# Performance work log

Hardware: AMD Instinct MI355X
Metric: run time of the kernel (lower is better)

Reference implementation:

```python
import jax, jax.numpy as jnp
import numpy as np

N_NODES = 50000
N_EDGES = 1600000
HIDDEN = 128
N_RBF = 50


def _linear_init(key, fan_in, fan_out):
    # mimic torch nn.Linear default init: U(-1/sqrt(fan_in), 1/sqrt(fan_in))
    kw, kb = jax.random.split(key)
    bound = 1.0 / np.sqrt(fan_in)
    W = jax.random.uniform(kw, (fan_in, fan_out), minval=-bound, maxval=bound, dtype=jnp.float32)
    b = jax.random.uniform(kb, (fan_out,), minval=-bound, maxval=bound, dtype=jnp.float32)
    return W, b


def setup_inputs() -> dict:
    key = jax.random.key(0)
    ks = jax.random.split(key, 9)
    x = jax.random.normal(ks[0], (N_NODES, HIDDEN), dtype=jnp.float32)
    edge_index = jax.random.randint(ks[1], (2, N_EDGES), 0, N_NODES, dtype=jnp.int32)
    edge_attr = jax.random.uniform(ks[2], (N_EDGES, N_RBF), dtype=jnp.float32)
    fW1, fb1 = _linear_init(ks[3], N_RBF, HIDDEN)
    fW2, fb2 = _linear_init(ks[4], HIDDEN, HIDDEN)
    dW, db = _linear_init(ks[5], HIDDEN, HIDDEN)
    uW1, ub1 = _linear_init(ks[6], HIDDEN, HIDDEN)
    uW2, ub2 = _linear_init(ks[7], HIDDEN, HIDDEN)
    return {
        "x": x, "edge_index": edge_index, "edge_attr": edge_attr,
        "fW1": fW1, "fb1": fb1, "fW2": fW2, "fb2": fb2,
        "dW": dW, "db": db,
        "uW1": uW1, "ub1": ub1, "uW2": uW2, "ub2": ub2,
    }


def reference(x, edge_index, edge_attr, fW1, fb1, fW2, fb2, dW, db, uW1, ub1, uW2, ub2):
    src, dst = edge_index[0], edge_index[1]
    # filter network: Linear -> SiLU -> Linear on edge RBF features [E, n_rbf] -> [E, H]
    filters = jax.nn.silu(edge_attr @ fW1 + fb1) @ fW2 + fb2
    # messages: dense(x[src]) * filters  [E, H]
    messages = (x[src] @ dW + db) * filters
    # scatter-add to destination nodes
    aggregated = jax.ops.segment_sum(messages, dst, num_segments=x.shape[0])
    # update MLP + residual
    upd = jax.nn.silu(aggregated @ uW1 + ub1) @ uW2 + ub2
    return x + upd
```

## Files before the change

### kernel.cpp

```cpp
#include <hip/hip_runtime.h>

#define H    128
#define RBF  50
#define K1   64
#define EB   64
#define NB   32
#define NBLK 1024

typedef _Float16 f16;
typedef _Float16 f16x8 __attribute__((ext_vector_type(8)));
typedef float    f32x4 __attribute__((ext_vector_type(4)));

#define HS_LD 136

__device__ __forceinline__ float silu_f(float a) {
    return a / (1.0f + __expf(-a));
}


__global__ __launch_bounds__(256) void prep1_kernel(
    const float* __restrict__ x, const float* __restrict__ dW,
    const float* __restrict__ db, f16* __restrict__ h, int N, int nH,
    const float* __restrict__ fW1, const float* __restrict__ fW2,
    f16* __restrict__ Wt1, f16* __restrict__ Wt2,
    const int* __restrict__ dst, int* __restrict__ counts, int E)
{
    __shared__ float xs[NB][H];
    const int tid = threadIdx.x;
    const int b   = blockIdx.x;

    if (b < nH) {
        const int n0 = b * NB;
        for (int idx = tid; idx < NB * H; idx += 256) {
            int r = idx >> 7, c = idx & (H - 1);
            int n = n0 + r;
            xs[r][c] = (n < N) ? x[(size_t)n * H + c] : 0.f;
        }
        __syncthreads();
        const int j  = tid & (H - 1);
        const int rb = (tid >> 7) * 16;
        float acc[16];
        const float bb = db[j];
#pragma unroll
        for (int r = 0; r < 16; ++r) acc[r] = bb;
        for (int kq = 0; kq < H / 4; ++kq) {
            const int k = kq * 4;
            const float w0 = dW[(k + 0) * H + j];
            const float w1 = dW[(k + 1) * H + j];
            const float w2 = dW[(k + 2) * H + j];
            const float w3 = dW[(k + 3) * H + j];
#pragma unroll
            for (int r = 0; r < 16; ++r) {
                const float4 v = *(const float4*)&xs[rb + r][k];
                acc[r] = fmaf(v.x, w0, fmaf(v.y, w1, fmaf(v.z, w2, fmaf(v.w, w3, acc[r]))));
            }
        }
#pragma unroll
        for (int r = 0; r < 16; ++r) {
            int n = n0 + rb + r;
            if (n < N) h[(size_t)n * H + j] = (f16)acc[r];
        }
    } else if (b < nH + 96) {
        int i = (b - nH) * 256 + tid;
        if (i < H * K1) {
            int n = i >> 6, k = i & (K1 - 1);
            Wt1[i] = (k < RBF) ? (f16)fW1[k * H + n] : (f16)0.f;
        }
        int jj = i - H * K1;
        if (jj >= 0 && jj < H * H) {
            int n = jj >> 7, k = jj & (H - 1);
            Wt2[jj] = (f16)fW2[k * H + n];
        }
    } else {
        const int hb  = b - nH - 96;
        const int hgd = gridDim.x - nH - 96;
        for (int i = hb * 256 + tid; i < E; i += hgd * 256)
            atomicAdd(&counts[dst[i]], 1);
    }
}


__global__ __launch_bounds__(256) void scan1_kernel(
    const int* __restrict__ counts, int* __restrict__ ofs, int* __restrict__ bsum, int N)
{
    __shared__ int s[256];
    const int t = threadIdx.x;
    const int g = blockIdx.x * 256 + t;
    int v = (g < N) ? counts[g] : 0;
    s[t] = v; __syncthreads();
    for (int off = 1; off < 256; off <<= 1) {
        int u = 0; if (t >= off) u = s[t - off];
        __syncthreads(); s[t] += u; __syncthreads();
    }
    if (g < N) ofs[g] = s[t] - v;
    if (t == 255) bsum[blockIdx.x] = s[255];
}
__global__ __launch_bounds__(256) void scan2_kernel(int* __restrict__ bsum, int nb)
{
    __shared__ int s[256];
    const int t = threadIdx.x;
    int v = (t < nb) ? bsum[t] : 0;
    s[t] = v; __syncthreads();
    for (int off = 1; off < 256; off <<= 1) {
        int u = 0; if (t >= off) u = s[t - off];
        __syncthreads(); s[t] += u; __syncthreads();
    }
    if (t < nb) bsum[t] = s[t] - v;
}
__global__ __launch_bounds__(256) void scan3_kernel(
    int* __restrict__ ofs, int* __restrict__ cursor, const int* __restrict__ bsum, int N)
{
    int g = blockIdx.x * 256 + threadIdx.x;
    if (g < N) {
        int v = ofs[g] + bsum[blockIdx.x];
        ofs[g] = v;
        cursor[g] = v;
    }
}

__global__ __launch_bounds__(256) void ranges_kernel(
    const int* __restrict__ ofs, int* __restrict__ nstart, int* __restrict__ estart,
    int N, int E, int B)
{
    int b = blockIdx.x * 256 + threadIdx.x;
    if (b > B) return;
    if (b == B) { nstart[B] = N; estart[B] = E; return; }
    long long cb = (long long)b * E / B;
    int lo = 0, hi = N;
    while (lo < hi) {
        int mid = (lo + hi) >> 1;
        int val = (mid < N) ? ofs[mid] : E;
        if (val < (int)cb) lo = mid + 1; else hi = mid;
    }
    nstart[b] = lo;
    estart[b] = (lo < N) ? ofs[lo] : E;
}

__global__ __launch_bounds__(256) void build_kernel(
    const float* __restrict__ ea, const int* __restrict__ src, const int* __restrict__ dst,
    int* __restrict__ cursor, int2* __restrict__ sd, f16* __restrict__ ea16, int E)
{
    for (int e = blockIdx.x * 256 + threadIdx.x; e < E; e += gridDim.x * 256) {
        const int d = dst[e];
        const int pos = atomicAdd(&cursor[d], 1);
        sd[pos] = make_int2(src[e], d);

        const float* rp = ea + (size_t)e * RBF;
        f16* op = ea16 + (size_t)pos * K1;
        f16x8 v[8];
#pragma unroll
        for (int q = 0; q < 6; ++q) {
            const float4 a = *(const float4*)(rp + q * 8);
            const float4 b = *(const float4*)(rp + q * 8 + 4);
            f16x8 t;
            t[0]=(f16)a.x; t[1]=(f16)a.y; t[2]=(f16)a.z; t[3]=(f16)a.w;
            t[4]=(f16)b.x; t[5]=(f16)b.y; t[6]=(f16)b.z; t[7]=(f16)b.w;
            v[q] = t;
        }
        {
            const float2 a = *(const float2*)(rp + 48);
            f16x8 t = {};
            t[0]=(f16)a.x; t[1]=(f16)a.y;
            v[6] = t;
        }
        v[7] = (f16x8){};
#pragma unroll
        for (int q = 0; q < 8; ++q) *(f16x8*)(op + q * 8) = v[q];
    }
}

__global__ __launch_bounds__(256, 4) void edge_fused_kernel(
    const f16* __restrict__ ea16, const int2* __restrict__ sd,
    const f16* __restrict__ Wt1, const f16* __restrict__ Wt2,
    const float* __restrict__ fb1, const float* __restrict__ fb2,
    const f16* __restrict__ h, float* __restrict__ out,
    const int* __restrict__ nstart, const int* __restrict__ estart)
{
    __shared__ __align__(16) f16 uni[8192];
    __shared__ __align__(16) f16 h_s[EB * HS_LD];
    __shared__ int src_s[2][EB];
    __shared__ int dst_s[2][EB];

    const int tid  = threadIdx.x;
    const int lane = tid & 63;
    const int wv   = tid >> 6;
    const int wr   = (wv >> 1) * 32;
    const int wc   = (wv & 1) * 64;
    const int fr   = lane & 15;
    const int qw   = lane >> 4;
    const int kb   = qw * 8;

    f16x8 B1[4][2];
    f16x8 B2[4][4];
    float b1v[4], b2v[4];
#pragma unroll
    for (int ct = 0; ct < 4; ++ct) {
        const int col = wc + ct * 16 + fr;
#pragma unroll
        for (int ks = 0; ks < 2; ++ks)
            B1[ct][ks] = *(const f16x8*)&Wt1[col * K1 + ks * 32 + kb];
#pragma unroll
        for (int ks = 0; ks < 4; ++ks)
            B2[ct][ks] = *(const f16x8*)&Wt2[col * H + ks * 32 + kb];
        b1v[ct] = fb1[col];
        b2v[ct] = fb2[col];
    }

    const int ns = nstart[blockIdx.x], ne = nstart[blockIdx.x + 1];
    const int e0 = estart[blockIdx.x], e1 = estart[blockIdx.x + 1];

    if (e0 >= e1) {
        for (int idx = tid; idx < (ne - ns) * H; idx += 256)
            out[(size_t)ns * H + idx] = 0.f;
        return;
    }

    const int col128 = tid & 127;
    int   curdst = ns;
    float accv   = 0.f;
    int   cur    = 0;

    if (tid < EB) {
        int idx = e0 + tid; idx = (idx < e1) ? idx : (e1 - 1);
        int2 v = sd[idx];
        src_s[0][tid] = v.x;
        dst_s[0][tid] = (e0 + tid < e1) ? v.y : ne;
    }
    __syncthreads();

    for (int tb = e0; tb < e1; tb += EB) {
        f16x8 eA0[2], eA1[2];
        {
            int r0 = tb + wr + fr;      r0 = (r0 < e1) ? r0 : (e1 - 1);
            int r1 = tb + wr + 16 + fr; r1 = (r1 < e1) ? r1 : (e1 - 1);
#pragma unroll
            for (int ks = 0; ks < 2; ++ks) {
                eA0[ks] = *(const f16x8*)&ea16[(size_t)r0 * K1 + (ks * 4 + qw) * 8];
                eA1[ks] = *(const f16x8*)&ea16[(size_t)r1 * K1 + (ks * 4 + qw) * 8];
            }
        }

        {
#pragma unroll
            for (int i = 0; i < 2; ++i) {
                const int row = (tid >> 3) + i * 32;
                const int ch  = tid & 7;
                const f16* hp = h + (size_t)src_s[cur][row] * H;
#pragma unroll
                for (int half = 0; half < 2; ++half)
                    *(f16x8*)&h_s[row * HS_LD + half * 64 + ch * 8] =
                        *(const f16x8*)(hp + half * 64 + ch * 8);
            }
        }
        __syncthreads();

        f32x4 acc1[2][4];
#pragma unroll
        for (int rt = 0; rt < 2; ++rt)
#pragma unroll
            for (int ct = 0; ct < 4; ++ct)
                acc1[rt][ct] = (f32x4){b1v[ct], b1v[ct], b1v[ct], b1v[ct]};
#pragma unroll
        for (int ks = 0; ks < 2; ++ks) {
#pragma unroll
            for (int ct = 0; ct < 4; ++ct) {
                acc1[0][ct] = __builtin_amdgcn_mfma_f32_16x16x32_f16(eA0[ks], B1[ct][ks], acc1[0][ct], 0, 0, 0);
                acc1[1][ct] = __builtin_amdgcn_mfma_f32_16x16x32_f16(eA1[ks], B1[ct][ks], acc1[1][ct], 0, 0, 0);
            }
        }

#pragma unroll
        for (int rt = 0; rt < 2; ++rt)
#pragma unroll
            for (int ct = 0; ct < 4; ++ct)
#pragma unroll
                for (int m = 0; m < 4; ++m) {
                    const int er = wr + rt * 16 + qw * 4 + m;
                    const int c  = wc + ct * 16 + fr;
                    *(f16*)((char*)uni + (size_t)(((c >> 3) * 64 + er) * 16 + (c & 7) * 2)) =
                        (f16)silu_f(acc1[rt][ct][m]);
                }
        __syncthreads();

        f32x4 acc2[2][4];
#pragma unroll
        for (int rt = 0; rt < 2; ++rt)
#pragma unroll
            for (int ct = 0; ct < 4; ++ct)
                acc2[rt][ct] = (f32x4){b2v[ct], b2v[ct], b2v[ct], b2v[ct]};
#pragma unroll
        for (int ks = 0; ks < 4; ++ks) {
            const f16x8 A0 = *(const f16x8*)((char*)uni + (size_t)(((ks * 4 + qw) * 64 + wr + fr) * 16));
            const f16x8 A1 = *(const f16x8*)((char*)uni + (size_t)(((ks * 4 + qw) * 64 + wr + 16 + fr) * 16));
#pragma unroll
            for (int ct = 0; ct < 4; ++ct) {
                acc2[0][ct] = __builtin_amdgcn_mfma_f32_16x16x32_f16(A0, B2[ct][ks], acc2[0][ct], 0, 0, 0);
                acc2[1][ct] = __builtin_amdgcn_mfma_f32_16x16x32_f16(A1, B2[ct][ks], acc2[1][ct], 0, 0, 0);
            }
        }

#pragma unroll
        for (int rt = 0; rt < 2; ++rt)
#pragma unroll
            for (int ct = 0; ct < 4; ++ct)
#pragma unroll
                for (int m = 0; m < 4; ++m) {
                    const int er = wr + rt * 16 + qw * 4 + m;
                    const int c  = wc + ct * 16 + fr;
                    f16* p = &h_s[er * HS_LD + c];
                    *p = (f16)((float)*p * acc2[rt][ct][m]);
                }
        __syncthreads();

        if (tid < 128) {
            const int* ds = dst_s[cur];
            for (int r = 0; r < EB; ++r) {
                const int d = ds[r];
                const float v = (float)h_s[r * HS_LD + col128];
                if (d != curdst) {
                    out[(size_t)curdst * H + col128] = accv;
                    for (int n = curdst + 1; n < d; ++n) out[(size_t)n * H + col128] = 0.f;
                    curdst = d; accv = 0.f;
                }
                if (d < ne) accv += v;
            }
        } else if (tid < 128 + EB) {
            const int r = tid - 128;
            int idx = tb + EB + r; idx = (idx < e1) ? idx : (e1 - 1);
            int2 v = sd[idx];
            src_s[cur ^ 1][r] = v.x;
            dst_s[cur ^ 1][r] = (tb + EB + r < e1) ? v.y : ne;
        }
        __syncthreads();

        cur ^= 1;
    }

    if (tid < 128 && curdst < ne) {
        out[(size_t)curdst * H + col128] = accv;
        for (int n = curdst + 1; n < ne; ++n) out[(size_t)n * H + col128] = 0.f;
    }
}

__global__ __launch_bounds__(256) void update_kernel(
    const float* __restrict__ x,
    const float* __restrict__ uW1, const float* __restrict__ ub1,
    const float* __restrict__ uW2, const float* __restrict__ ub2,
    float* __restrict__ out, int N)
{
    __shared__ float as[NB][H];
    __shared__ float ts[NB][H];
    const int tid = threadIdx.x;
    const int n0  = blockIdx.x * NB;
    for (int idx = tid; idx < NB * H; idx += 256) {
        int r = idx >> 7, c = idx & (H - 1);
        int n = n0 + r;
        as[r][c] = (n < N) ? out[(size_t)n * H + c] : 0.f;
    }
    __syncthreads();
    const int j  = tid & (H - 1);
    const int rb = (tid >> 7) * 16;
    float acc[16];
    {
        const float b1 = ub1[j];
#pragma unroll
        for (int r = 0; r < 16; ++r) acc[r] = b1;
    }
    for (int kq = 0; kq < H / 4; ++kq) {
        const int k = kq * 4;
        const float w0 = uW1[(k + 0) * H + j];
        const float w1 = uW1[(k + 1) * H + j];
        const float w2 = uW1[(k + 2) * H + j];
        const float w3 = uW1[(k + 3) * H + j];
#pragma unroll
        for (int r = 0; r < 16; ++r) {
            const float4 v = *(const float4*)&as[rb + r][k];
            acc[r] = fmaf(v.x, w0, fmaf(v.y, w1, fmaf(v.z, w2, fmaf(v.w, w3, acc[r]))));
        }
    }
#pragma unroll
    for (int r = 0; r < 16; ++r) ts[rb + r][j] = silu_f(acc[r]);
    __syncthreads();
    {
        const float b2 = ub2[j];
#pragma unroll
        for (int r = 0; r < 16; ++r) acc[r] = b2;
    }
    for (int kq = 0; kq < H / 4; ++kq) {
        const int k = kq * 4;
        const float w0 = uW2[(k + 0) * H + j];
        const float w1 = uW2[(k + 1) * H + j];
        const float w2 = uW2[(k + 2) * H + j];
        const float w3 = uW2[(k + 3) * H + j];
#pragma unroll
        for (int r = 0; r < 16; ++r) {
            const float4 v = *(const float4*)&ts[rb + r][k];
            acc[r] = fmaf(v.x, w0, fmaf(v.y, w1, fmaf(v.z, w2, fmaf(v.w, w3, acc[r]))));
        }
    }
#pragma unroll
    for (int r = 0; r < 16; ++r) {
        int n = n0 + rb + r;
        if (n < N) out[(size_t)n * H + j] = x[(size_t)n * H + j] + acc[r];
    }
}

extern "C" void kernel_launch(void* const* d_in, const int* in_sizes, int n_in,
                              void* d_out, int out_size, void* d_ws, size_t ws_size,
                              hipStream_t stream) {
    const float* x   = (const float*)d_in[0];
    const int*   ei  = (const int*)  d_in[1];
    const float* ea  = (const float*)d_in[2];
    const float* fW1 = (const float*)d_in[3];
    const float* fb1 = (const float*)d_in[4];
    const float* fW2 = (const float*)d_in[5];
    const float* fb2 = (const float*)d_in[6];
    const float* dW  = (const float*)d_in[7];
    const float* db  = (const float*)d_in[8];
    const float* uW1 = (const float*)d_in[9];
    const float* ub1 = (const float*)d_in[10];
    const float* uW2 = (const float*)d_in[11];
    const float* ub2 = (const float*)d_in[12];

    float* out = (float*)d_out;
    const int N = in_sizes[0] / H;
    const int E = in_sizes[1] / 2;
    const int* src = ei;
    const int* dst = ei + E;

    char* ws = (char*)d_ws;
    size_t off = 0;
    auto alloc = [&](size_t bytes) { void* p = ws + off; off = (off + bytes + 255) & ~(size_t)255; return p; };
    f16*  h      = (f16*) alloc((size_t)N * H * sizeof(f16));
    f16*  Wt1    = (f16*) alloc((size_t)H * K1 * sizeof(f16));
    f16*  Wt2    = (f16*) alloc((size_t)H * H * sizeof(f16));
    int*  counts = (int*) alloc((size_t)N * sizeof(int));
    int*  ofs    = (int*) alloc((size_t)N * sizeof(int));
    int*  cursor = (int*) alloc((size_t)N * sizeof(int));
    int*  bsum   = (int*) alloc(256 * sizeof(int));
    int*  nstart = (int*) alloc((size_t)(NBLK + 1) * sizeof(int));
    int*  estart = (int*) alloc((size_t)(NBLK + 1) * sizeof(int));
    int2* sd     = (int2*)alloc((size_t)E * sizeof(int2));
    f16*  ea16   = (f16*) alloc((size_t)E * K1 * sizeof(f16));

    const int nH    = (N + NB - 1) / NB;
    const int nscan = (N + 255) / 256;

    hipMemsetAsync(counts, 0, (size_t)N * sizeof(int), stream);

    prep1_kernel<<<nH + 96 + 2048, 256, 0, stream>>>(
        x, dW, db, h, N, nH, fW1, fW2, Wt1, Wt2, dst, counts, E);

    scan1_kernel<<<nscan, 256, 0, stream>>>(counts, ofs, bsum, N);
    scan2_kernel<<<1, 256, 0, stream>>>(bsum, nscan);
    scan3_kernel<<<nscan, 256, 0, stream>>>(ofs, cursor, bsum, N);

    ranges_kernel<<<(NBLK + 256) / 256, 256, 0, stream>>>(ofs, nstart, estart, N, E, NBLK);

    build_kernel<<<2048, 256, 0, stream>>>(ea, src, dst, cursor, sd, ea16, E);

    edge_fused_kernel<<<NBLK, 256, 0, stream>>>(
        ea16, sd, Wt1, Wt2, fb1, fb2, h, out, nstart, estart);

    update_kernel<<<nH, 256, 0, stream>>>(
        x, uW1, ub1, uW2, ub2, out, N);
}
```

Baseline: 939.2 us.

## Pack src/dst into padded edge feature rows and prefetch edge tiles via LDS

The build kernel now stores each edge's src and dst indices in the unused padding slot of the 64-wide fp16 edge feature row, which removes the separate int2 sorted index array and its extra write and read. The fused edge kernel loads whole edge rows cooperatively, pulls src/dst out with shuffles, stages features in LDS for the first GEMM, and prefetches the next tile into registers one iteration ahead. Output writes are batched in groups of four nodes with nontemporal stores, and input reads use nontemporal hints. This adds an extra barrier per tile and more complex flush logic for sparse destination runs.

```diff
diff --git a/kernel.cpp b/kernel.cpp
--- a/kernel.cpp
+++ b/kernel.cpp
@@ -10,6 +10,8 @@
 typedef _Float16 f16;
 typedef _Float16 f16x8 __attribute__((ext_vector_type(8)));
 typedef float    f32x4 __attribute__((ext_vector_type(4)));
+typedef float    fv4   __attribute__((ext_vector_type(4)));
+typedef float    fv2   __attribute__((ext_vector_type(2)));
 
 #define HS_LD 136
 
@@ -138,39 +140,45 @@
 
 __global__ __launch_bounds__(256) void build_kernel(
     const float* __restrict__ ea, const int* __restrict__ src, const int* __restrict__ dst,
-    int* __restrict__ cursor, int2* __restrict__ sd, f16* __restrict__ ea16, int E)
+    int* __restrict__ cursor, f16* __restrict__ ea16, int E)
 {
     for (int e = blockIdx.x * 256 + threadIdx.x; e < E; e += gridDim.x * 256) {
-        const int d = dst[e];
+        const int d  = dst[e];
+        const int sV = src[e];
         const int pos = atomicAdd(&cursor[d], 1);
-        sd[pos] = make_int2(src[e], d);
 
         const float* rp = ea + (size_t)e * RBF;
         f16* op = ea16 + (size_t)pos * K1;
         f16x8 v[8];
 #pragma unroll
         for (int q = 0; q < 6; ++q) {
-            const float4 a = *(const float4*)(rp + q * 8);
-            const float4 b = *(const float4*)(rp + q * 8 + 4);
+            const fv4 a = __builtin_nontemporal_load((const fv4*)(rp + q * 8));
+            const fv4 b = __builtin_nontemporal_load((const fv4*)(rp + q * 8 + 4));
             f16x8 t;
             t[0]=(f16)a.x; t[1]=(f16)a.y; t[2]=(f16)a.z; t[3]=(f16)a.w;
             t[4]=(f16)b.x; t[5]=(f16)b.y; t[6]=(f16)b.z; t[7]=(f16)b.w;
             v[q] = t;
         }
         {
-            const float2 a = *(const float2*)(rp + 48);
+            const fv2 a = __builtin_nontemporal_load((const fv2*)(rp + 48));
             f16x8 t = {};
             t[0]=(f16)a.x; t[1]=(f16)a.y;
             v[6] = t;
         }
-        v[7] = (f16x8){};
-#pragma unroll
-        for (int q = 0; q < 8; ++q) *(f16x8*)(op + q * 8) = v[q];
+        {
+            f16x8 t = {};
+            ((int*)&t)[0] = sV;
+            ((int*)&t)[1] = d;
+            v[7] = t;
+        }
+#pragma unroll
+        for (int q = 0; q < 8; ++q)
+            __builtin_nontemporal_store(v[q], (f16x8*)(op + q * 8));
     }
 }
 
 __global__ __launch_bounds__(256, 4) void edge_fused_kernel(
-    const f16* __restrict__ ea16, const int2* __restrict__ sd,
+    const f16* __restrict__ ea16,
     const f16* __restrict__ Wt1, const f16* __restrict__ Wt2,
     const float* __restrict__ fb1, const float* __restrict__ fb2,
     const f16* __restrict__ h, float* __restrict__ out,
@@ -178,8 +186,7 @@
 {
     __shared__ __align__(16) f16 uni[8192];
     __shared__ __align__(16) f16 h_s[EB * HS_LD];
-    __shared__ int src_s[2][EB];
-    __shared__ int dst_s[2][EB];
+    __shared__ int dst_s[EB];
 
     const int tid  = threadIdx.x;
     const int lane = tid & 63;
@@ -190,6 +197,8 @@
     const int qw   = lane >> 4;
     const int kb   = qw * 8;
 
+    const int ch = tid & 7;
+
     f16x8 B1[4][2];
     f16x8 B2[4][4];
     float b1v[4], b2v[4];
@@ -209,50 +218,58 @@
     const int ns = nstart[blockIdx.x], ne = nstart[blockIdx.x + 1];
     const int e0 = estart[blockIdx.x], e1 = estart[blockIdx.x + 1];
 
+    const int col128 = tid & 127;
+
     if (e0 >= e1) {
         for (int idx = tid; idx < (ne - ns) * H; idx += 256)
             out[(size_t)ns * H + idx] = 0.f;
         return;
     }
 
-    const int col128 = tid & 127;
     int   curdst = ns;
     float accv   = 0.f;
-    int   cur    = 0;
-
-    if (tid < EB) {
-        int idx = e0 + tid; idx = (idx < e1) ? idx : (e1 - 1);
-        int2 v = sd[idx];
-        src_s[0][tid] = v.x;
-        dst_s[0][tid] = (e0 + tid < e1) ? v.y : ne;
-    }
-    __syncthreads();
+    int   wbase  = ns & ~3;
+    float wc0 = 0.f, wc1 = 0.f, wc2 = 0.f, wc3 = 0.f;
+
+#define FLUSH4 do { \
+    if (wbase     >= ns && wbase     < ne) __builtin_nontemporal_store(wc0, &out[(size_t)(wbase    ) * H + col128]); \
+    if (wbase + 1 >= ns && wbase + 1 < ne) __builtin_nontemporal_store(wc1, &out[(size_t)(wbase + 1) * H + col128]); \
+    if (wbase + 2 >= ns && wbase + 2 < ne) __builtin_nontemporal_store(wc2, &out[(size_t)(wbase + 2) * H + col128]); \
+    if (wbase + 3 >= ns && wbase + 3 < ne) __builtin_nontemporal_store(wc3, &out[(size_t)(wbase + 3) * H + col128]); \
+    wc0 = wc1 = wc2 = wc3 = 0.f; } while (0)
+
+    f16x8 evC[2], evN[2];
+#pragma unroll
+    for (int i = 0; i < 2; ++i) {
+        const int row = (tid >> 3) + i * 32;
+        int pe = e0 + row; pe = (pe < e1) ? pe : (e1 - 1);
+        evC[i] = __builtin_nontemporal_load((const f16x8*)(ea16 + (size_t)pe * K1 + ch * 8));
+    }
 
     for (int tb = e0; tb < e1; tb += EB) {
-        f16x8 eA0[2], eA1[2];
-        {
-            int r0 = tb + wr + fr;      r0 = (r0 < e1) ? r0 : (e1 - 1);
-            int r1 = tb + wr + 16 + fr; r1 = (r1 < e1) ? r1 : (e1 - 1);
-#pragma unroll
-            for (int ks = 0; ks < 2; ++ks) {
-                eA0[ks] = *(const f16x8*)&ea16[(size_t)r0 * K1 + (ks * 4 + qw) * 8];
-                eA1[ks] = *(const f16x8*)&ea16[(size_t)r1 * K1 + (ks * 4 + qw) * 8];
-            }
-        }
-
-        {
-#pragma unroll
-            for (int i = 0; i < 2; ++i) {
-                const int row = (tid >> 3) + i * 32;
-                const int ch  = tid & 7;
-                const f16* hp = h + (size_t)src_s[cur][row] * H;
-#pragma unroll
-                for (int half = 0; half < 2; ++half)
-                    *(f16x8*)&h_s[row * HS_LD + half * 64 + ch * 8] =
-                        *(const f16x8*)(hp + half * 64 + ch * 8);
-            }
-        }
-        __syncthreads();
+#pragma unroll
+        for (int i = 0; i < 2; ++i) {
+            const int row = (tid >> 3) + i * 32;
+            const int sp = ((int*)&evC[i])[0];
+            const int dp = ((int*)&evC[i])[1];
+            const int srcv = __shfl(sp, lane | 7);
+            const int dstv = __shfl(dp, lane | 7);
+            f16x8 w = evC[i];
+            if (ch == 7) { w[0] = (f16)0.f; w[1] = (f16)0.f; w[2] = (f16)0.f; w[3] = (f16)0.f; }
+            *(f16x8*)((char*)uni + (size_t)((ch * 64 + row) * 16)) = w;
+            const f16* hp = h + (size_t)srcv * H;
+            *(f16x8*)&h_s[row * HS_LD + ch * 8]      = *(const f16x8*)(hp + ch * 8);
+            *(f16x8*)&h_s[row * HS_LD + 64 + ch * 8] = *(const f16x8*)(hp + 64 + ch * 8);
+            if (ch == 7) dst_s[row] = (tb + row < e1) ? dstv : ne;
+        }
+        __syncthreads();
+
+#pragma unroll
+        for (int i = 0; i < 2; ++i) {
+            const int row = (tid >> 3) + i * 32;
+            int pe = tb + EB + row; pe = (pe < e1) ? pe : (e1 - 1);
+            evN[i] = __builtin_nontemporal_load((const f16x8*)(ea16 + (size_t)pe * K1 + ch * 8));
+        }
 
         f32x4 acc1[2][4];
 #pragma unroll
@@ -262,12 +279,15 @@
                 acc1[rt][ct] = (f32x4){b1v[ct], b1v[ct], b1v[ct], b1v[ct]};
 #pragma unroll
         for (int ks = 0; ks < 2; ++ks) {
+            const f16x8 A0 = *(const f16x8*)((char*)uni + (size_t)(((ks * 4 + qw) * 64 + wr + fr) * 16));
+            const f16x8 A1 = *(const f16x8*)((char*)uni + (size_t)(((ks * 4 + qw) * 64 + wr + 16 + fr) * 16));
 #pragma unroll
             for (int ct = 0; ct < 4; ++ct) {
-                acc1[0][ct] = __builtin_amdgcn_mfma_f32_16x16x32_f16(eA0[ks], B1[ct][ks], acc1[0][ct], 0, 0, 0);
-                acc1[1][ct] = __builtin_amdgcn_mfma_f32_16x16x32_f16(eA1[ks], B1[ct][ks], acc1[1][ct], 0, 0, 0);
+                acc1[0][ct] = __builtin_amdgcn_mfma_f32_16x16x32_f16(A0, B1[ct][ks], acc1[0][ct], 0, 0, 0);
+                acc1[1][ct] = __builtin_amdgcn_mfma_f32_16x16x32_f16(A1, B1[ct][ks], acc1[1][ct], 0, 0, 0);
             }
         }
+        __syncthreads();
 
 #pragma unroll
         for (int rt = 0; rt < 2; ++rt)
@@ -313,33 +333,42 @@
         __syncthreads();
 
         if (tid < 128) {
-            const int* ds = dst_s[cur];
             for (int r = 0; r < EB; ++r) {
-                const int d = ds[r];
+                const int d = dst_s[r];
                 const float v = (float)h_s[r * HS_LD + col128];
                 if (d != curdst) {
-                    out[(size_t)curdst * H + col128] = accv;
-                    for (int n = curdst + 1; n < d; ++n) out[(size_t)n * H + col128] = 0.f;
+                    if (curdst < ne) {
+                        while (curdst >= wbase + 4) { FLUSH4; wbase += 4; }
+                        const int sl = curdst - wbase;
+                        if      (sl == 0) wc0 = accv;
+                        else if (sl == 1) wc1 = accv;
+                        else if (sl == 2) wc2 = accv;
+                        else              wc3 = accv;
+                    }
                     curdst = d; accv = 0.f;
                 }
                 if (d < ne) accv += v;
             }
-        } else if (tid < 128 + EB) {
-            const int r = tid - 128;
-            int idx = tb + EB + r; idx = (idx < e1) ? idx : (e1 - 1);
-            int2 v = sd[idx];
-            src_s[cur ^ 1][r] = v.x;
-            dst_s[cur ^ 1][r] = (tb + EB + r < e1) ? v.y : ne;
-        }
-        __syncthreads();
-
-        cur ^= 1;
-    }
-
-    if (tid < 128 && curdst < ne) {
-        out[(size_t)curdst * H + col128] = accv;
-        for (int n = curdst + 1; n < ne; ++n) out[(size_t)n * H + col128] = 0.f;
-    }
+        }
+        __syncthreads();
+
+        evC[0] = evN[0]; evC[1] = evN[1];
+    }
+
+    if (tid < 128) {
+        if (curdst < ne) {
+            while (curdst >= wbase + 4) { FLUSH4; wbase += 4; }
+            const int sl = curdst - wbase;
+            if      (sl == 0) wc0 = accv;
+            else if (sl == 1) wc1 = accv;
+            else if (sl == 2) wc2 = accv;
+            else              wc3 = accv;
+        }
+        FLUSH4;
+        for (int n = wbase + 4; n < ne; ++n)
+            __builtin_nontemporal_store(0.f, &out[(size_t)n * H + col128]);
+    }
+#undef FLUSH4
 }
 
 __global__ __launch_bounds__(256) void update_kernel(
@@ -440,7 +469,6 @@
     int*  bsum   = (int*) alloc(256 * sizeof(int));
     int*  nstart = (int*) alloc((size_t)(NBLK + 1) * sizeof(int));
     int*  estart = (int*) alloc((size_t)(NBLK + 1) * sizeof(int));
-    int2* sd     = (int2*)alloc((size_t)E * sizeof(int2));
     f16*  ea16   = (f16*) alloc((size_t)E * K1 * sizeof(f16));
 
     const int nH    = (N + NB - 1) / NB;
@@ -457,10 +485,10 @@
 
     ranges_kernel<<<(NBLK + 256) / 256, 256, 0, stream>>>(ofs, nstart, estart, N, E, NBLK);
 
-    build_kernel<<<2048, 256, 0, stream>>>(ea, src, dst, cursor, sd, ea16, E);
+    build_kernel<<<2048, 256, 0, stream>>>(ea, src, dst, cursor, ea16, E);
 
     edge_fused_kernel<<<NBLK, 256, 0, stream>>>(
-        ea16, sd, Wt1, Wt2, fb1, fb2, h, out, nstart, estart);
+        ea16, Wt1, Wt2, fb1, fb2, h, out, nstart, estart);
 
     update_kernel<<<nH, 256, 0, stream>>>(
         x, uW1, ub1, uW2, ub2, out, N);
```

New measurement: 1.157 ms. 23.2% more time.
